# Performance work log

Measured on AMD Instinct MI355X. Metric: run time of the kernel, lower is better.

Reference implementation:

```python
import jax, jax.numpy as jnp
import numpy as np

B, C, H, W = 16, 256, 64, 64
NUM_HEADS = 4
GROUPS = 8
EPS = 1e-5


def setup_inputs() -> dict:
    key = jax.random.key(0)
    ks = jax.random.split(key, 7)
    x = jax.random.normal(ks[0], (B, C, H, W), dtype=jnp.float32)
    # GroupNorm affine params (torch default: weight=1, bias=0; randomize slightly for a stronger test)
    norm_w = jnp.ones((C,), jnp.float32) + 0.1 * jax.random.normal(ks[1], (C,), jnp.float32)
    norm_b = 0.1 * jax.random.normal(ks[2], (C,), jnp.float32)
    # 1x1 convs == channel GEMMs; kaiming-uniform-ish init scale
    s = 1.0 / np.sqrt(C)
    qkv_w = jax.random.uniform(ks[3], (3 * C, C), jnp.float32, -s, s)
    qkv_b = jax.random.uniform(ks[4], (3 * C,), jnp.float32, -s, s)
    proj_w = jax.random.uniform(ks[5], (C, C), jnp.float32, -s, s)
    proj_b = jax.random.uniform(ks[6], (C,), jnp.float32, -s, s)
    return {"x": x, "norm_w": norm_w, "norm_b": norm_b,
            "qkv_w": qkv_w, "qkv_b": qkv_b, "proj_w": proj_w, "proj_b": proj_b}


def reference(x, norm_w, norm_b, qkv_w, qkv_b, proj_w, proj_b):
    b, c, h, w = x.shape
    nh = NUM_HEADS
    dh = c // nh
    n = h * w
    # GroupNorm(8, C)
    xg = x.reshape(b, GROUPS, c // GROUPS, h, w)
    mean = xg.mean(axis=(2, 3, 4), keepdims=True)
    var = xg.var(axis=(2, 3, 4), keepdims=True)
    xn = ((xg - mean) * jax.lax.rsqrt(var + EPS)).reshape(b, c, h, w)
    xn = xn * norm_w[None, :, None, None] + norm_b[None, :, None, None]
    # QKV 1x1 conv as channel GEMM
    qkv = jnp.einsum('bchw,oc->bohw', xn, qkv_w) + qkv_b[None, :, None, None]
    qkv = qkv.reshape(b, 3, nh, dh, n)
    q, k, v = qkv[:, 0], qkv[:, 1], qkv[:, 2]  # each (B, nh, dh, N)
    scale = dh ** (-0.5)
    # Faithful to original einsum labeling: contracts over spatial axis,
    # attention matrix is over the HEADS axis: attn (B, dh, nh, nh)
    attn = jnp.einsum('bnhd,bmhd->bhnm', q * scale, k)
    attn = jax.nn.softmax(attn, axis=-1)
    out = jnp.einsum('bhnm,bmhd->bnhd', attn, v).reshape(b, c, h, w)
    return jnp.einsum('bchw,oc->bohw', out, proj_w) + proj_b[None, :, None, None] + x
```

## Files before the change

### kernel.cpp

```cpp
#include <hip/hip_runtime.h>
#include <stdint.h>

#define BB 16
#define CC 256
#define PP 4096
#define CPG 32

typedef __attribute__((ext_vector_type(4))) float f32x4;
typedef __attribute__((ext_vector_type(8))) short bf16x8;

static __device__ __forceinline__ float bf2f(unsigned short u) {
    union { uint32_t i; float f; } w; w.i = ((uint32_t)u) << 16; return w.f;
}
static __device__ __forceinline__ unsigned short f2bf(float f) {
    union { float f; uint32_t i; } w; w.f = f;
    uint32_t u = w.i;
    uint32_t r = u + 0x7FFFu + ((u >> 16) & 1u);
    return (unsigned short)(r >> 16);
}

static __device__ __forceinline__ void gl2lds16(const void* g, void* l) {
    __builtin_amdgcn_global_load_lds(
        (const __attribute__((address_space(1))) void*)g,
        (__attribute__((address_space(3))) void*)l, 16, 0, 0);
}

__global__ void gn_partial_k(const float* __restrict__ x, float* __restrict__ part) {
    int bg = blockIdx.x >> 2, chunk = blockIdx.x & 3;
    const f32x4* v = (const f32x4*)(x + (size_t)bg * (CPG * PP) + (size_t)chunk * (CPG * PP / 4));
    float s = 0.f, ss = 0.f;
    for (int i = threadIdx.x; i < (CPG * PP / 4 / 4); i += 256) {
        f32x4 t = v[i];
        s  += t.x + t.y + t.z + t.w;
        ss += t.x * t.x + t.y * t.y + t.z * t.z + t.w * t.w;
    }
    for (int off = 32; off > 0; off >>= 1) {
        s  += __shfl_down(s, off);
        ss += __shfl_down(ss, off);
    }
    __shared__ float ls[4], lss[4];
    int wv = threadIdx.x >> 6;
    if ((threadIdx.x & 63) == 0) { ls[wv] = s; lss[wv] = ss; }
    __syncthreads();
    if (threadIdx.x == 0) {
        part[blockIdx.x * 2 + 0] = ls[0] + ls[1] + ls[2] + ls[3];
        part[blockIdx.x * 2 + 1] = lss[0] + lss[1] + lss[2] + lss[3];
    }
}

__global__ void gn_final_k(const float* __restrict__ part, const float* __restrict__ nw,
                           const float* __restrict__ nb, float* __restrict__ a_s,
                           float* __restrict__ b_s) {
    int bg = threadIdx.x;
    float S = 0.f, SS = 0.f;
    for (int i = 0; i < 4; i++) { S += part[(bg * 4 + i) * 2]; SS += part[(bg * 4 + i) * 2 + 1]; }
    const float inv = 1.0f / (float)(CPG * PP);
    float mean = S * inv;
    float var = SS * inv - mean * mean;
    float rstd = rsqrtf(var + 1e-5f);
    int b = bg >> 3, g = bg & 7;
    for (int j = 0; j < CPG; j++) {
        int c = g * CPG + j;
        float w = nw[c];
        a_s[b * CC + c] = rstd * w;
        b_s[b * CC + c] = nb[c] - mean * rstd * w;
    }
}

__global__ void cvt_bf16_k(const float* __restrict__ in, unsigned short* __restrict__ out, int n) {
    int i = blockIdx.x * 256 + threadIdx.x;
    if (i < n) out[i] = f2bf(in[i]);
}

__global__ void xnt_k(const float* __restrict__ x, const float* __restrict__ a_s,
                      const float* __restrict__ b_s, unsigned short* __restrict__ xnT) {
    int pt = blockIdx.x & 63, ct = (blockIdx.x >> 6) & 3, b = blockIdx.x >> 8;
    int c0 = ct * 64, p0 = pt * 64;
    __shared__ unsigned short T[64][66];
    int t = threadIdx.x;
    int cl = t >> 4, pl4 = (t & 15) * 4;
    for (int i = 0; i < 4; i++) {
        int c = c0 + i * 16 + cl;
        float a = a_s[b * CC + c], sh = b_s[b * CC + c];
        f32x4 v = *(const f32x4*)(x + ((size_t)b * CC + c) * PP + p0 + pl4);
        T[i * 16 + cl][pl4 + 0] = f2bf(a * v.x + sh);
        T[i * 16 + cl][pl4 + 1] = f2bf(a * v.y + sh);
        T[i * 16 + cl][pl4 + 2] = f2bf(a * v.z + sh);
        T[i * 16 + cl][pl4 + 3] = f2bf(a * v.w + sh);
    }
    __syncthreads();
    int pl = t >> 2, c16 = (t & 3) * 16;
    union { unsigned short h[16]; uint4 u[2]; } buf;
    for (int j = 0; j < 16; j++) buf.h[j] = T[c16 + j][pl];
    unsigned short* dst = xnT + ((size_t)b * PP + p0 + pl) * CC + c0 + c16;
    *(uint4*)dst       = buf.u[0];
    *(uint4*)(dst + 8) = buf.u[1];
}

static __device__ __forceinline__ void gemm_core(const unsigned short* __restrict__ Rg,
                                                 const unsigned short* __restrict__ Cg,
                                                 f32x4 (&acc)[4][4]) {
    __shared__ unsigned short Rs[128][32];
    __shared__ unsigned short Cs[128][32];
    int t = threadIdx.x;
    int lane = t & 63, wave = t >> 6;
    int wm = wave >> 1, wn = wave & 1;
    int lr = lane & 15, lq = lane >> 4;
    int srow = t >> 2, sk8 = (t & 3) * 8;
    for (int mi = 0; mi < 4; mi++)
        for (int ni = 0; ni < 4; ni++) {
            acc[mi][ni][0] = 0.f; acc[mi][ni][1] = 0.f;
            acc[mi][ni][2] = 0.f; acc[mi][ni][3] = 0.f;
        }
    const unsigned short* gr0 = Rg + (size_t)srow * 256 + sk8;
    const unsigned short* gr1 = gr0 + (size_t)64 * 256;
    const unsigned short* gc0 = Cg + (size_t)srow * 256 + sk8;
    const unsigned short* gc1 = gc0 + (size_t)64 * 256;
    char* lr0 = (char*)&Rs[0][0] + t * 16;
    char* lr1 = lr0 + 4096;
    char* lc0 = (char*)&Cs[0][0] + t * 16;
    char* lc1 = lc0 + 4096;
    for (int k0 = 0; k0 < 256; k0 += 32) {
        __syncthreads();
        gl2lds16(gr0 + k0, lr0);
        gl2lds16(gr1 + k0, lr1);
        gl2lds16(gc0 + k0, lc0);
        gl2lds16(gc1 + k0, lc1);
        __syncthreads();
        bf16x8 af[4], bfr[4];
        for (int mi = 0; mi < 4; mi++) af[mi]  = *(const bf16x8*)&Rs[wm * 64 + mi * 16 + lr][lq * 8];
        for (int ni = 0; ni < 4; ni++) bfr[ni] = *(const bf16x8*)&Cs[wn * 64 + ni * 16 + lr][lq * 8];
        for (int mi = 0; mi < 4; mi++)
            for (int ni = 0; ni < 4; ni++)
                acc[mi][ni] = __builtin_amdgcn_mfma_f32_16x16x32_bf16(af[mi], bfr[ni], acc[mi][ni], 0, 0, 0);
    }
}

__global__ __launch_bounds__(256) void qkv_gemm_k(const unsigned short* __restrict__ Wq,
                                                  const unsigned short* __restrict__ xnT,
                                                  const float* __restrict__ qkv_b,
                                                  unsigned short* __restrict__ qk,
                                                  unsigned short* __restrict__ vT) {
    int nt = blockIdx.x & 31;
    int rest = blockIdx.x >> 5;
    int mt = rest % 6;
    int b  = rest / 6;
    int o0 = mt * 128, p0 = nt * 128;
    int t = threadIdx.x, lane = t & 63, wave = t >> 6;
    int wm = wave >> 1, wn = wave & 1, lr = lane & 15, lq = lane >> 4;
    f32x4 acc[4][4];
    if (o0 < 512) {
        gemm_core(xnT + ((size_t)b * PP + p0) * 256, Wq + (size_t)o0 * 256, acc);
        for (int mi = 0; mi < 4; mi++) {
            int p4 = p0 + wm * 64 + mi * 16 + lq * 4;
            for (int ni = 0; ni < 4; ni++) {
                int o = o0 + wn * 64 + ni * 16 + lr;
                float bias = qkv_b[o];
                ushort4 u;
                u.x = f2bf(acc[mi][ni][0] + bias);
                u.y = f2bf(acc[mi][ni][1] + bias);
                u.z = f2bf(acc[mi][ni][2] + bias);
                u.w = f2bf(acc[mi][ni][3] + bias);
                *(ushort4*)(qk + ((size_t)b * 512 + o) * PP + p4) = u;
            }
        }
    } else {
        gemm_core(Wq + (size_t)o0 * 256, xnT + ((size_t)b * PP + p0) * 256, acc);
        for (int mi = 0; mi < 4; mi++) {
            int c4 = (o0 - 512) + wm * 64 + mi * 16 + lq * 4;
            for (int ni = 0; ni < 4; ni++) {
                int p = p0 + wn * 64 + ni * 16 + lr;
                ushort4 u;
                u.x = f2bf(acc[mi][ni][0] + qkv_b[512 + c4 + 0]);
                u.y = f2bf(acc[mi][ni][1] + qkv_b[512 + c4 + 1]);
                u.z = f2bf(acc[mi][ni][2] + qkv_b[512 + c4 + 2]);
                u.w = f2bf(acc[mi][ni][3] + qkv_b[512 + c4 + 3]);
                *(ushort4*)(vT + ((size_t)b * PP + p) * CC + c4) = u;
            }
        }
    }
}

__global__ void scores_k(const unsigned short* __restrict__ qk, float* __restrict__ attn) {
    int b = blockIdx.x >> 6, hh = blockIdx.x & 63;
    int t = threadIdx.x, lane = t & 63, wave = t >> 6;
    float acc[16];
    for (int i = 0; i < 16; i++) acc[i] = 0.f;
    const unsigned short* qb = qk + (size_t)b * 512 * PP + (size_t)hh * PP;
    for (int p = t * 8; p < PP; p += 2048) {
        float qv[4][8], kv[4][8];
        for (int n = 0; n < 4; n++) {
            uint4 u = *(const uint4*)(qb + (size_t)n * 64 * PP + p);
            const unsigned short* hs = (const unsigned short*)&u;
            for (int j = 0; j < 8; j++) qv[n][j] = bf2f(hs[j]);
        }
        for (int m = 0; m < 4; m++) {
            uint4 u = *(const uint4*)(qb + (size_t)(256 + m * 64) * PP + p);
            const unsigned short* hs = (const unsigned short*)&u;
            for (int j = 0; j < 8; j++) kv[m][j] = bf2f(hs[j]);
        }
        for (int n = 0; n < 4; n++)
            for (int m = 0; m < 4; m++) {
                float s = 0.f;
                for (int j = 0; j < 8; j++) s += qv[n][j] * kv[m][j];
                acc[n * 4 + m] += s;
            }
    }
    __shared__ float red[4][16];
    __shared__ float sfin[16];
    for (int i = 0; i < 16; i++) {
        float v = acc[i];
        for (int off = 32; off > 0; off >>= 1) v += __shfl_down(v, off);
        if (lane == 0) red[wave][i] = v;
    }
    __syncthreads();
    if (t < 16) sfin[t] = red[0][t] + red[1][t] + red[2][t] + red[3][t];
    __syncthreads();
    if (t < 4) {
        float v0 = sfin[t * 4 + 0] * 0.125f, v1 = sfin[t * 4 + 1] * 0.125f;
        float v2 = sfin[t * 4 + 2] * 0.125f, v3 = sfin[t * 4 + 3] * 0.125f;
        float mx = fmaxf(fmaxf(v0, v1), fmaxf(v2, v3));
        float e0 = expf(v0 - mx), e1 = expf(v1 - mx), e2 = expf(v2 - mx), e3 = expf(v3 - mx);
        float inv = 1.0f / (e0 + e1 + e2 + e3);
        float* dst = attn + ((size_t)(b * 64 + hh) * 4 + t) * 4;
        dst[0] = e0 * inv; dst[1] = e1 * inv; dst[2] = e2 * inv; dst[3] = e3 * inv;
    }
}

__global__ void make_wp_k(const float* __restrict__ proj_w, const float* __restrict__ attn,
                          unsigned short* __restrict__ Wp) {
    int t = threadIdx.x;
    int o = blockIdx.x & 255, b = blockIdx.x >> 8;
    int m = t >> 6, hh = t & 63;
    float s = 0.f;
    for (int n = 0; n < 4; n++)
        s += proj_w[o * 256 + n * 64 + hh] * attn[((size_t)(b * 64 + hh) * 4 + n) * 4 + m];
    Wp[((size_t)b * 256 + o) * 256 + t] = f2bf(s);
}

__global__ __launch_bounds__(256) void final_gemm_k(const unsigned short* __restrict__ Wp,
                                                    const unsigned short* __restrict__ vT,
                                                    const float* __restrict__ proj_b,
                                                    const float* __restrict__ x,
                                                    float* __restrict__ out) {
    int nt = blockIdx.x & 31;
    int rest = blockIdx.x >> 5;
    int mt = rest & 1;
    int b  = rest >> 1;
    int o0 = mt * 128, p0 = nt * 128;
    f32x4 acc[4][4];
    gemm_core(vT + ((size_t)b * PP + p0) * 256, Wp + ((size_t)b * 256 + o0) * 256, acc);
    int t = threadIdx.x, lane = t & 63, wave = t >> 6;
    int wm = wave >> 1, wn = wave & 1, lr = lane & 15, lq = lane >> 4;
    for (int mi = 0; mi < 4; mi++) {
        int p4 = p0 + wm * 64 + mi * 16 + lq * 4;
        for (int ni = 0; ni < 4; ni++) {
            int o = o0 + wn * 64 + ni * 16 + lr;
            size_t idx = ((size_t)b * CC + o) * PP + p4;
            float bias = proj_b[o];
            f32x4 xv = *(const f32x4*)(x + idx);
            f32x4 r;
            r[0] = acc[mi][ni][0] + bias + xv[0];
            r[1] = acc[mi][ni][1] + bias + xv[1];
            r[2] = acc[mi][ni][2] + bias + xv[2];
            r[3] = acc[mi][ni][3] + bias + xv[3];
            *(f32x4*)(out + idx) = r;
        }
    }
}

extern "C" void kernel_launch(void* const* d_in, const int* in_sizes, int n_in,
                              void* d_out, int out_size, void* d_ws, size_t ws_size,
                              hipStream_t stream) {
    const float* x      = (const float*)d_in[0];
    const float* norm_w = (const float*)d_in[1];
    const float* norm_b = (const float*)d_in[2];
    const float* qkv_w  = (const float*)d_in[3];
    const float* qkv_b  = (const float*)d_in[4];
    const float* proj_w = (const float*)d_in[5];
    const float* proj_b = (const float*)d_in[6];
    float* out = (float*)d_out;

    char* ws = (char*)d_ws;
    size_t off = 0;
    auto alloc = [&](size_t bytes) {
        void* p = ws + off;
        off += (bytes + 255) & ~(size_t)255;
        return p;
    };
    float* part = (float*)alloc(512 * 2 * sizeof(float));
    float* a_s  = (float*)alloc(BB * CC * sizeof(float));
    float* b_s  = (float*)alloc(BB * CC * sizeof(float));
    float* attn = (float*)alloc((size_t)BB * 64 * 16 * sizeof(float));
    unsigned short* Wqb = (unsigned short*)alloc((size_t)768 * 256 * 2);
    unsigned short* Wp  = (unsigned short*)alloc((size_t)BB * 256 * 256 * 2);
    unsigned short* xnT = (unsigned short*)alloc((size_t)BB * PP * CC * 2);
    unsigned short* qk  = (unsigned short*)alloc((size_t)BB * 512 * PP * 2);
    unsigned short* vT  = (unsigned short*)alloc((size_t)BB * PP * CC * 2);

    gn_partial_k<<<512, 256, 0, stream>>>(x, part);
    gn_final_k<<<1, 128, 0, stream>>>(part, norm_w, norm_b, a_s, b_s);
    cvt_bf16_k<<<768, 256, 0, stream>>>(qkv_w, Wqb, 768 * 256);
    xnt_k<<<4096, 256, 0, stream>>>(x, a_s, b_s, xnT);
    qkv_gemm_k<<<16 * 6 * 32, 256, 0, stream>>>(Wqb, xnT, qkv_b, qk, vT);
    scores_k<<<16 * 64, 256, 0, stream>>>(qk, attn);
    make_wp_k<<<16 * 256, 256, 0, stream>>>(proj_w, attn, Wp);
    final_gemm_k<<<16 * 2 * 32, 256, 0, stream>>>(Wp, vT, proj_b, x, out);
}
```

Before: 283.5 us.

## Compute attention scores via Gram matrix of normalized input instead of Q/K GEMM

Removes materializing Q and K (512 channels × 4096 positions per batch) and instead computes the channel Gram matrix xn·xnᵀ, then folds Wq and Wk algebraically to get the head-axis scores, with bias terms handled through per-channel sums. The QKV GEMM becomes a V-only GEMM, and the Gram is split over position chunks with a separate reduction. It also adds an XOR swizzle to LDS tiles in the shared GEMM core to reduce bank conflicts, and restructures GroupNorm stats per channel. Costs include writing an extra channel-major copy of xn, a large fp32 partial-Gram buffer, and bf16 rounding of the Gram, which may affect accuracy.

```diff
diff --git a/kernel.cpp b/kernel.cpp
--- a/kernel.cpp
+++ b/kernel.cpp
@@ -4,7 +4,6 @@
 #define BB 16
 #define CC 256
 #define PP 4096
-#define CPG 32
 
 typedef __attribute__((ext_vector_type(4))) float f32x4;
 typedef __attribute__((ext_vector_type(8))) short bf16x8;
@@ -18,6 +17,9 @@
     uint32_t r = u + 0x7FFFu + ((u >> 16) & 1u);
     return (unsigned short)(r >> 16);
 }
+static __device__ __forceinline__ float dot4(f32x4 a, f32x4 b) {
+    return a.x * b.x + a.y * b.y + a.z * b.z + a.w * b.w;
+}
 
 static __device__ __forceinline__ void gl2lds16(const void* g, void* l) {
     __builtin_amdgcn_global_load_lds(
@@ -25,46 +27,48 @@
         (__attribute__((address_space(3))) void*)l, 16, 0, 0);
 }
 
-__global__ void gn_partial_k(const float* __restrict__ x, float* __restrict__ part) {
-    int bg = blockIdx.x >> 2, chunk = blockIdx.x & 3;
-    const f32x4* v = (const f32x4*)(x + (size_t)bg * (CPG * PP) + (size_t)chunk * (CPG * PP / 4));
+__global__ void gn_partial_k(const float* __restrict__ x, float* __restrict__ Sx,
+                             float* __restrict__ Sxx) {
+    int ch0 = blockIdx.x * 8;
+    int t = threadIdx.x;
+    int lc = t >> 5, l32 = t & 31;
+    int ch = ch0 + lc;
+    const f32x4* v = (const f32x4*)(x + (size_t)ch * PP);
     float s = 0.f, ss = 0.f;
-    for (int i = threadIdx.x; i < (CPG * PP / 4 / 4); i += 256) {
-        f32x4 t = v[i];
-        s  += t.x + t.y + t.z + t.w;
-        ss += t.x * t.x + t.y * t.y + t.z * t.z + t.w * t.w;
-    }
-    for (int off = 32; off > 0; off >>= 1) {
-        s  += __shfl_down(s, off);
-        ss += __shfl_down(ss, off);
-    }
-    __shared__ float ls[4], lss[4];
-    int wv = threadIdx.x >> 6;
-    if ((threadIdx.x & 63) == 0) { ls[wv] = s; lss[wv] = ss; }
+    for (int i = l32; i < PP / 4; i += 32) {
+        f32x4 tv = v[i];
+        s  += tv.x + tv.y + tv.z + tv.w;
+        ss += tv.x * tv.x + tv.y * tv.y + tv.z * tv.z + tv.w * tv.w;
+    }
+    for (int off = 16; off > 0; off >>= 1) {
+        s  += __shfl_down(s, off, 32);
+        ss += __shfl_down(ss, off, 32);
+    }
+    if (l32 == 0) { Sx[ch] = s; Sxx[ch] = ss; }
+}
+
+__global__ void gn_final_k(const float* __restrict__ Sx, const float* __restrict__ Sxx,
+                           const float* __restrict__ nw, const float* __restrict__ nb,
+                           float* __restrict__ a_s, float* __restrict__ b_s,
+                           float* __restrict__ s_vec) {
+    int b = blockIdx.x, c = threadIdx.x;
+    __shared__ float lsx[256], lsxx[256];
+    float mySx = Sx[b * CC + c];
+    lsx[c] = mySx; lsxx[c] = Sxx[b * CC + c];
     __syncthreads();
-    if (threadIdx.x == 0) {
-        part[blockIdx.x * 2 + 0] = ls[0] + ls[1] + ls[2] + ls[3];
-        part[blockIdx.x * 2 + 1] = lss[0] + lss[1] + lss[2] + lss[3];
-    }
-}
-
-__global__ void gn_final_k(const float* __restrict__ part, const float* __restrict__ nw,
-                           const float* __restrict__ nb, float* __restrict__ a_s,
-                           float* __restrict__ b_s) {
-    int bg = threadIdx.x;
+    int g0 = (c >> 5) << 5;
     float S = 0.f, SS = 0.f;
-    for (int i = 0; i < 4; i++) { S += part[(bg * 4 + i) * 2]; SS += part[(bg * 4 + i) * 2 + 1]; }
-    const float inv = 1.0f / (float)(CPG * PP);
+    for (int j = 0; j < 32; j++) { S += lsx[g0 + j]; SS += lsxx[g0 + j]; }
+    const float inv = 1.0f / 131072.0f;
     float mean = S * inv;
     float var = SS * inv - mean * mean;
     float rstd = rsqrtf(var + 1e-5f);
-    int b = bg >> 3, g = bg & 7;
-    for (int j = 0; j < CPG; j++) {
-        int c = g * CPG + j;
-        float w = nw[c];
-        a_s[b * CC + c] = rstd * w;
-        b_s[b * CC + c] = nb[c] - mean * rstd * w;
-    }
+    float w = nw[c];
+    float a = rstd * w;
+    float sh = nb[c] - mean * rstd * w;
+    a_s[b * CC + c] = a;
+    b_s[b * CC + c] = sh;
+    s_vec[b * CC + c] = a * mySx + 4096.0f * sh;
 }
 
 __global__ void cvt_bf16_k(const float* __restrict__ in, unsigned short* __restrict__ out, int n) {
@@ -73,7 +77,8 @@
 }
 
 __global__ void xnt_k(const float* __restrict__ x, const float* __restrict__ a_s,
-                      const float* __restrict__ b_s, unsigned short* __restrict__ xnT) {
+                      const float* __restrict__ b_s, unsigned short* __restrict__ xnT,
+                      unsigned short* __restrict__ xnC) {
     int pt = blockIdx.x & 63, ct = (blockIdx.x >> 6) & 3, b = blockIdx.x >> 8;
     int c0 = ct * 64, p0 = pt * 64;
     __shared__ unsigned short T[64][66];
@@ -83,10 +88,16 @@
         int c = c0 + i * 16 + cl;
         float a = a_s[b * CC + c], sh = b_s[b * CC + c];
         f32x4 v = *(const f32x4*)(x + ((size_t)b * CC + c) * PP + p0 + pl4);
-        T[i * 16 + cl][pl4 + 0] = f2bf(a * v.x + sh);
-        T[i * 16 + cl][pl4 + 1] = f2bf(a * v.y + sh);
-        T[i * 16 + cl][pl4 + 2] = f2bf(a * v.z + sh);
-        T[i * 16 + cl][pl4 + 3] = f2bf(a * v.w + sh);
+        ushort4 u;
+        u.x = f2bf(a * v.x + sh);
+        u.y = f2bf(a * v.y + sh);
+        u.z = f2bf(a * v.z + sh);
+        u.w = f2bf(a * v.w + sh);
+        T[i * 16 + cl][pl4 + 0] = u.x;
+        T[i * 16 + cl][pl4 + 1] = u.y;
+        T[i * 16 + cl][pl4 + 2] = u.z;
+        T[i * 16 + cl][pl4 + 3] = u.w;
+        *(ushort4*)(xnC + ((size_t)b * CC + c) * PP + p0 + pl4) = u;
     }
     __syncthreads();
     int pl = t >> 2, c16 = (t & 3) * 16;
@@ -99,6 +110,7 @@
 
 static __device__ __forceinline__ void gemm_core(const unsigned short* __restrict__ Rg,
                                                  const unsigned short* __restrict__ Cg,
+                                                 int kLen, int rstride,
                                                  f32x4 (&acc)[4][4]) {
     __shared__ unsigned short Rs[128][32];
     __shared__ unsigned short Cs[128][32];
@@ -106,123 +118,155 @@
     int lane = t & 63, wave = t >> 6;
     int wm = wave >> 1, wn = wave & 1;
     int lr = lane & 15, lq = lane >> 4;
-    int srow = t >> 2, sk8 = (t & 3) * 8;
+    int srow = t >> 2;
+    int ssl = (((t & 3) ^ ((t >> 3) & 3))) * 8;
+    int fsw = (lr >> 1) & 3;
     for (int mi = 0; mi < 4; mi++)
         for (int ni = 0; ni < 4; ni++) {
             acc[mi][ni][0] = 0.f; acc[mi][ni][1] = 0.f;
             acc[mi][ni][2] = 0.f; acc[mi][ni][3] = 0.f;
         }
-    const unsigned short* gr0 = Rg + (size_t)srow * 256 + sk8;
-    const unsigned short* gr1 = gr0 + (size_t)64 * 256;
-    const unsigned short* gc0 = Cg + (size_t)srow * 256 + sk8;
-    const unsigned short* gc1 = gc0 + (size_t)64 * 256;
-    char* lr0 = (char*)&Rs[0][0] + t * 16;
-    char* lr1 = lr0 + 4096;
-    char* lc0 = (char*)&Cs[0][0] + t * 16;
-    char* lc1 = lc0 + 4096;
-    for (int k0 = 0; k0 < 256; k0 += 32) {
+    const unsigned short* gr0 = Rg + (size_t)srow * rstride + ssl;
+    const unsigned short* gr1 = gr0 + (size_t)64 * rstride;
+    const unsigned short* gc0 = Cg + (size_t)srow * rstride + ssl;
+    const unsigned short* gc1 = gc0 + (size_t)64 * rstride;
+    char* dr0 = (char*)&Rs[0][0] + t * 16;
+    char* dr1 = dr0 + 4096;
+    char* dc0 = (char*)&Cs[0][0] + t * 16;
+    char* dc1 = dc0 + 4096;
+    for (int k0 = 0; k0 < kLen; k0 += 32) {
         __syncthreads();
-        gl2lds16(gr0 + k0, lr0);
-        gl2lds16(gr1 + k0, lr1);
-        gl2lds16(gc0 + k0, lc0);
-        gl2lds16(gc1 + k0, lc1);
+        gl2lds16(gr0 + k0, dr0);
+        gl2lds16(gr1 + k0, dr1);
+        gl2lds16(gc0 + k0, dc0);
+        gl2lds16(gc1 + k0, dc1);
         __syncthreads();
         bf16x8 af[4], bfr[4];
-        for (int mi = 0; mi < 4; mi++) af[mi]  = *(const bf16x8*)&Rs[wm * 64 + mi * 16 + lr][lq * 8];
-        for (int ni = 0; ni < 4; ni++) bfr[ni] = *(const bf16x8*)&Cs[wn * 64 + ni * 16 + lr][lq * 8];
+        for (int mi = 0; mi < 4; mi++)
+            af[mi]  = *(const bf16x8*)&Rs[wm * 64 + mi * 16 + lr][(lq ^ fsw) * 8];
+        for (int ni = 0; ni < 4; ni++)
+            bfr[ni] = *(const bf16x8*)&Cs[wn * 64 + ni * 16 + lr][(lq ^ fsw) * 8];
         for (int mi = 0; mi < 4; mi++)
             for (int ni = 0; ni < 4; ni++)
                 acc[mi][ni] = __builtin_amdgcn_mfma_f32_16x16x32_bf16(af[mi], bfr[ni], acc[mi][ni], 0, 0, 0);
     }
 }
 
-__global__ __launch_bounds__(256) void qkv_gemm_k(const unsigned short* __restrict__ Wq,
-                                                  const unsigned short* __restrict__ xnT,
-                                                  const float* __restrict__ qkv_b,
-                                                  unsigned short* __restrict__ qk,
-                                                  unsigned short* __restrict__ vT) {
+__global__ __launch_bounds__(256) void v_gemm_k(const unsigned short* __restrict__ Wvb,
+                                                const unsigned short* __restrict__ xnT,
+                                                const float* __restrict__ qkv_b,
+                                                unsigned short* __restrict__ vT) {
     int nt = blockIdx.x & 31;
     int rest = blockIdx.x >> 5;
-    int mt = rest % 6;
-    int b  = rest / 6;
-    int o0 = mt * 128, p0 = nt * 128;
+    int mt = rest & 1;
+    int b  = rest >> 1;
+    int c0 = mt * 128, p0 = nt * 128;
+    f32x4 acc[4][4];
+    gemm_core(Wvb + (size_t)c0 * 256, xnT + ((size_t)b * PP + p0) * 256, 256, 256, acc);
     int t = threadIdx.x, lane = t & 63, wave = t >> 6;
     int wm = wave >> 1, wn = wave & 1, lr = lane & 15, lq = lane >> 4;
+    for (int mi = 0; mi < 4; mi++) {
+        int c4 = c0 + wm * 64 + mi * 16 + lq * 4;
+        f32x4 bias = *(const f32x4*)(qkv_b + 512 + c4);
+        for (int ni = 0; ni < 4; ni++) {
+            int p = p0 + wn * 64 + ni * 16 + lr;
+            ushort4 u;
+            u.x = f2bf(acc[mi][ni][0] + bias.x);
+            u.y = f2bf(acc[mi][ni][1] + bias.y);
+            u.z = f2bf(acc[mi][ni][2] + bias.z);
+            u.w = f2bf(acc[mi][ni][3] + bias.w);
+            *(ushort4*)(vT + ((size_t)b * PP + p) * CC + c4) = u;
+        }
+    }
+}
+
+__global__ __launch_bounds__(256) void gram_k(const unsigned short* __restrict__ xnC,
+                                              float* __restrict__ Gpart) {
+    int pc  = blockIdx.x & 7;
+    int t12 = (blockIdx.x >> 3) & 3;
+    int b   = blockIdx.x >> 5;
+    int t1 = (t12 >> 1) * 128;
+    int t2 = (t12 & 1) * 128;
     f32x4 acc[4][4];
-    if (o0 < 512) {
-        gemm_core(xnT + ((size_t)b * PP + p0) * 256, Wq + (size_t)o0 * 256, acc);
-        for (int mi = 0; mi < 4; mi++) {
-            int p4 = p0 + wm * 64 + mi * 16 + lq * 4;
-            for (int ni = 0; ni < 4; ni++) {
-                int o = o0 + wn * 64 + ni * 16 + lr;
-                float bias = qkv_b[o];
-                ushort4 u;
-                u.x = f2bf(acc[mi][ni][0] + bias);
-                u.y = f2bf(acc[mi][ni][1] + bias);
-                u.z = f2bf(acc[mi][ni][2] + bias);
-                u.w = f2bf(acc[mi][ni][3] + bias);
-                *(ushort4*)(qk + ((size_t)b * 512 + o) * PP + p4) = u;
-            }
-        }
-    } else {
-        gemm_core(Wq + (size_t)o0 * 256, xnT + ((size_t)b * PP + p0) * 256, acc);
-        for (int mi = 0; mi < 4; mi++) {
-            int c4 = (o0 - 512) + wm * 64 + mi * 16 + lq * 4;
-            for (int ni = 0; ni < 4; ni++) {
-                int p = p0 + wn * 64 + ni * 16 + lr;
-                ushort4 u;
-                u.x = f2bf(acc[mi][ni][0] + qkv_b[512 + c4 + 0]);
-                u.y = f2bf(acc[mi][ni][1] + qkv_b[512 + c4 + 1]);
-                u.z = f2bf(acc[mi][ni][2] + qkv_b[512 + c4 + 2]);
-                u.w = f2bf(acc[mi][ni][3] + qkv_b[512 + c4 + 3]);
-                *(ushort4*)(vT + ((size_t)b * PP + p) * CC + c4) = u;
-            }
-        }
-    }
-}
-
-__global__ void scores_k(const unsigned short* __restrict__ qk, float* __restrict__ attn) {
-    int b = blockIdx.x >> 6, hh = blockIdx.x & 63;
+    gemm_core(xnC + ((size_t)b * CC + t2) * PP + pc * 512,
+              xnC + ((size_t)b * CC + t1) * PP + pc * 512, 512, PP, acc);
     int t = threadIdx.x, lane = t & 63, wave = t >> 6;
-    float acc[16];
-    for (int i = 0; i < 16; i++) acc[i] = 0.f;
-    const unsigned short* qb = qk + (size_t)b * 512 * PP + (size_t)hh * PP;
-    for (int p = t * 8; p < PP; p += 2048) {
-        float qv[4][8], kv[4][8];
-        for (int n = 0; n < 4; n++) {
-            uint4 u = *(const uint4*)(qb + (size_t)n * 64 * PP + p);
-            const unsigned short* hs = (const unsigned short*)&u;
-            for (int j = 0; j < 8; j++) qv[n][j] = bf2f(hs[j]);
-        }
+    int wm = wave >> 1, wn = wave & 1, lr = lane & 15, lq = lane >> 4;
+    float* dst = Gpart + ((size_t)(pc * 16 + b)) * 65536;
+    for (int mi = 0; mi < 4; mi++) {
+        int c2q = t2 + wm * 64 + mi * 16 + lq * 4;
+        for (int ni = 0; ni < 4; ni++) {
+            int c1 = t1 + wn * 64 + ni * 16 + lr;
+            *(f32x4*)(dst + (size_t)c1 * 256 + c2q) = acc[mi][ni];
+        }
+    }
+}
+
+__global__ void greduce_k(const float* __restrict__ Gpart, unsigned short* __restrict__ Gb) {
+    int i = blockIdx.x * 256 + threadIdx.x;
+    float s = 0.f;
+    for (int pc = 0; pc < 8; pc++) s += Gpart[(size_t)pc * 16 * 65536 + i];
+    Gb[i] = f2bf(s);
+}
+
+__global__ __launch_bounds__(256) void u_gemm_k(const unsigned short* __restrict__ Gb,
+                                                const unsigned short* __restrict__ Wqkvb,
+                                                float* __restrict__ UT) {
+    int t12 = blockIdx.x & 3, b = blockIdx.x >> 2;
+    int t1 = (t12 >> 1) * 128;
+    int t2 = (t12 & 1) * 128;
+    f32x4 acc[4][4];
+    gemm_core(Gb + ((size_t)b * 256 + t1) * 256,
+              Wqkvb + (size_t)(256 + t2) * 256, 256, 256, acc);
+    int t = threadIdx.x, lane = t & 63, wave = t >> 6;
+    int wm = wave >> 1, wn = wave & 1, lr = lane & 15, lq = lane >> 4;
+    for (int mi = 0; mi < 4; mi++) {
+        int c1q = t1 + wm * 64 + mi * 16 + lq * 4;
+        for (int ni = 0; ni < 4; ni++) {
+            int kr = t2 + wn * 64 + ni * 16 + lr;
+            *(f32x4*)(UT + ((size_t)b * 256 + kr) * 256 + c1q) = acc[mi][ni];
+        }
+    }
+}
+
+__global__ void scoresfin_k(const float* __restrict__ qkv_w, const float* __restrict__ qkv_b,
+                            const float* __restrict__ UT, const float* __restrict__ s_vec,
+                            float* __restrict__ attn) {
+    int h = blockIdx.x & 63, b = blockIdx.x >> 6;
+    int l = threadIdx.x;
+    int c = l * 4;
+    f32x4 sv = *(const f32x4*)(s_vec + b * CC + c);
+    f32x4 wq[4], wk[4], ut[4];
+    for (int n = 0; n < 4; n++) wq[n] = *(const f32x4*)(qkv_w + (size_t)(n * 64 + h) * 256 + c);
+    for (int m = 0; m < 4; m++) wk[m] = *(const f32x4*)(qkv_w + (size_t)(256 + m * 64 + h) * 256 + c);
+    for (int m = 0; m < 4; m++) ut[m] = *(const f32x4*)(UT + ((size_t)b * 256 + m * 64 + h) * 256 + c);
+    float red[24];
+    for (int n = 0; n < 4; n++)
+        for (int m = 0; m < 4; m++) red[n * 4 + m] = dot4(wq[n], ut[m]);
+    for (int n = 0; n < 4; n++) red[16 + n] = dot4(wq[n], sv);
+    for (int m = 0; m < 4; m++) red[20 + m] = dot4(wk[m], sv);
+    #pragma unroll
+    for (int i = 0; i < 24; i++)
+        for (int off = 32; off > 0; off >>= 1)
+            red[i] += __shfl_xor(red[i], off);
+    __shared__ float sred[24];
+    if (l == 0)
+        for (int i = 0; i < 24; i++) sred[i] = red[i];
+    __syncthreads();
+    if (l < 4) {
+        int n = l;
+        float bq = qkv_b[n * 64 + h];
+        float dqn = sred[16 + n];
+        float lg[4];
         for (int m = 0; m < 4; m++) {
-            uint4 u = *(const uint4*)(qb + (size_t)(256 + m * 64) * PP + p);
-            const unsigned short* hs = (const unsigned short*)&u;
-            for (int j = 0; j < 8; j++) kv[m][j] = bf2f(hs[j]);
-        }
-        for (int n = 0; n < 4; n++)
-            for (int m = 0; m < 4; m++) {
-                float s = 0.f;
-                for (int j = 0; j < 8; j++) s += qv[n][j] * kv[m][j];
-                acc[n * 4 + m] += s;
-            }
-    }
-    __shared__ float red[4][16];
-    __shared__ float sfin[16];
-    for (int i = 0; i < 16; i++) {
-        float v = acc[i];
-        for (int off = 32; off > 0; off >>= 1) v += __shfl_down(v, off);
-        if (lane == 0) red[wave][i] = v;
-    }
-    __syncthreads();
-    if (t < 16) sfin[t] = red[0][t] + red[1][t] + red[2][t] + red[3][t];
-    __syncthreads();
-    if (t < 4) {
-        float v0 = sfin[t * 4 + 0] * 0.125f, v1 = sfin[t * 4 + 1] * 0.125f;
-        float v2 = sfin[t * 4 + 2] * 0.125f, v3 = sfin[t * 4 + 3] * 0.125f;
-        float mx = fmaxf(fmaxf(v0, v1), fmaxf(v2, v3));
-        float e0 = expf(v0 - mx), e1 = expf(v1 - mx), e2 = expf(v2 - mx), e3 = expf(v3 - mx);
+            float bk = qkv_b[256 + m * 64 + h];
+            lg[m] = 0.125f * (sred[n * 4 + m] + bq * sred[20 + m] + bk * dqn + 4096.0f * bq * bk);
+        }
+        float mx = fmaxf(fmaxf(lg[0], lg[1]), fmaxf(lg[2], lg[3]));
+        float e0 = expf(lg[0] - mx), e1 = expf(lg[1] - mx);
+        float e2 = expf(lg[2] - mx), e3 = expf(lg[3] - mx);
         float inv = 1.0f / (e0 + e1 + e2 + e3);
-        float* dst = attn + ((size_t)(b * 64 + hh) * 4 + t) * 4;
+        float* dst = attn + ((size_t)(b * 64 + h) * 4 + n) * 4;
         dst[0] = e0 * inv; dst[1] = e1 * inv; dst[2] = e2 * inv; dst[3] = e3 * inv;
     }
 }
@@ -249,7 +293,7 @@
     int b  = rest >> 1;
     int o0 = mt * 128, p0 = nt * 128;
     f32x4 acc[4][4];
-    gemm_core(vT + ((size_t)b * PP + p0) * 256, Wp + ((size_t)b * 256 + o0) * 256, acc);
+    gemm_core(vT + ((size_t)b * PP + p0) * 256, Wp + ((size_t)b * 256 + o0) * 256, 256, 256, acc);
     int t = threadIdx.x, lane = t & 63, wave = t >> 6;
     int wm = wave >> 1, wn = wave & 1, lr = lane & 15, lq = lane >> 4;
     for (int mi = 0; mi < 4; mi++) {
@@ -288,22 +332,30 @@
         off += (bytes + 255) & ~(size_t)255;
         return p;
     };
-    float* part = (float*)alloc(512 * 2 * sizeof(float));
-    float* a_s  = (float*)alloc(BB * CC * sizeof(float));
-    float* b_s  = (float*)alloc(BB * CC * sizeof(float));
-    float* attn = (float*)alloc((size_t)BB * 64 * 16 * sizeof(float));
-    unsigned short* Wqb = (unsigned short*)alloc((size_t)768 * 256 * 2);
-    unsigned short* Wp  = (unsigned short*)alloc((size_t)BB * 256 * 256 * 2);
-    unsigned short* xnT = (unsigned short*)alloc((size_t)BB * PP * CC * 2);
-    unsigned short* qk  = (unsigned short*)alloc((size_t)BB * 512 * PP * 2);
-    unsigned short* vT  = (unsigned short*)alloc((size_t)BB * PP * CC * 2);
-
-    gn_partial_k<<<512, 256, 0, stream>>>(x, part);
-    gn_final_k<<<1, 128, 0, stream>>>(part, norm_w, norm_b, a_s, b_s);
-    cvt_bf16_k<<<768, 256, 0, stream>>>(qkv_w, Wqb, 768 * 256);
-    xnt_k<<<4096, 256, 0, stream>>>(x, a_s, b_s, xnT);
-    qkv_gemm_k<<<16 * 6 * 32, 256, 0, stream>>>(Wqb, xnT, qkv_b, qk, vT);
-    scores_k<<<16 * 64, 256, 0, stream>>>(qk, attn);
-    make_wp_k<<<16 * 256, 256, 0, stream>>>(proj_w, attn, Wp);
-    final_gemm_k<<<16 * 2 * 32, 256, 0, stream>>>(Wp, vT, proj_b, x, out);
-}
+    float* Sx    = (float*)alloc(BB * CC * sizeof(float));
+    float* Sxx   = (float*)alloc(BB * CC * sizeof(float));
+    float* a_s   = (float*)alloc(BB * CC * sizeof(float));
+    float* b_s   = (float*)alloc(BB * CC * sizeof(float));
+    float* s_vec = (float*)alloc(BB * CC * sizeof(float));
+    float* attn  = (float*)alloc((size_t)BB * 64 * 16 * sizeof(float));
+    unsigned short* Wqkvb = (unsigned short*)alloc((size_t)768 * 256 * 2);
+    unsigned short* Wp    = (unsigned short*)alloc((size_t)BB * 256 * 256 * 2);
+    unsigned short* Gb    = (unsigned short*)alloc((size_t)BB * 65536 * 2);
+    float*          UT    = (float*)alloc((size_t)BB * 65536 * 4);
+    float*          Gpart = (float*)alloc((size_t)8 * BB * 65536 * 4);
+    unsigned short* xnT   = (unsigned short*)alloc((size_t)BB * PP * CC * 2);
+    unsigned short* xnC   = (unsigned short*)alloc((size_t)BB * PP * CC * 2);
+    unsigned short* vT    = (unsigned short*)alloc((size_t)BB * PP * CC * 2);
+
+    gn_partial_k<<<BB * CC / 8, 256, 0, stream>>>(x, Sx, Sxx);
+    gn_final_k<<<BB, 256, 0, stream>>>(Sx, Sxx, norm_w, norm_b, a_s, b_s, s_vec);
+    cvt_bf16_k<<<768, 256, 0, stream>>>(qkv_w, Wqkvb, 768 * 256);
+    xnt_k<<<4096, 256, 0, stream>>>(x, a_s, b_s, xnT, xnC);
+    v_gemm_k<<<BB * 2 * 32, 256, 0, stream>>>(Wqkvb + 512 * 256, xnT, qkv_b, vT);
+    gram_k<<<BB * 4 * 8, 256, 0, stream>>>(xnC, Gpart);
+    greduce_k<<<BB * 65536 / 256, 256, 0, stream>>>(Gpart, Gb);
+    u_gemm_k<<<BB * 4, 256, 0, stream>>>(Gb, Wqkvb, UT);
+    scoresfin_k<<<BB * 64, 64, 0, stream>>>(qkv_w, qkv_b, UT, s_vec, attn);
+    make_wp_k<<<BB * 256, 256, 0, stream>>>(proj_w, attn, Wp);
+    final_gemm_k<<<BB * 2 * 32, 256, 0, stream>>>(Wp, vT, proj_b, x, out);
+}
```

Result: faster. 270.2 us (-4.7%).
